# Kernel tuning notes

Hardware: AMD Instinct MI355X
Metric: run time of the kernel (lower is better)

Reference implementation:

```python
import jax, jax.numpy as jnp
import numpy as np


def setup_inputs() -> dict:
    key = jax.random.key(0)
    ks = jax.random.split(key, 8)
    B, L, D = 8, 4096, 1024
    s = 1.0 / np.sqrt(D)  # torch Linear default init scale (approx)
    return {
        "x": jax.random.normal(ks[0], (B, L, D), dtype=jnp.float32),
        "hidden": jax.random.normal(ks[1], (B, D), dtype=jnp.float32),
        "W_f": jax.random.normal(ks[2], (D, D), dtype=jnp.float32) * s,
        "b_f": jnp.zeros((D,), dtype=jnp.float32),
        "W_i": jax.random.normal(ks[3], (D, D), dtype=jnp.float32) * s,
        "b_i": jnp.zeros((D,), dtype=jnp.float32),
        "W_o": jax.random.normal(ks[4], (D, D), dtype=jnp.float32) * s,
        "b_o": jnp.zeros((D,), dtype=jnp.float32),
    }


def reference(x, hidden, W_f, b_f, W_i, b_i, W_o, b_o):
    # x: [B, L, D], hidden: [B, D]
    D = x.shape[-1]
    lin = jnp.linspace(0.0, 1.0, D, dtype=x.dtype)  # per-channel gate scale
    remember = jax.nn.sigmoid(jnp.einsum('bld,ed->ble', x, W_f) + b_f) * lin
    forget = 1.0 - remember
    inp = jnp.tanh(jnp.einsum('bld,ed->ble', x, W_i) + b_i) * remember

    # linear recurrence h_t = forget_t * h_{t-1} + inp_t  via parallel scan
    def combine(c1, c2):
        a1, u1 = c1
        a2, u2 = c2
        return (a1 * a2, a2 * u1 + u2)

    cumprod_forget, h_inner = jax.lax.associative_scan(combine, (forget, inp), axis=1)
    h = h_inner + hidden[:, None, :] * cumprod_forget  # inject initial hidden state
    y = jnp.einsum('bld,ed->ble', h, W_o) + b_o
    return y, h
```

## Files before the change

kernel.cpp:

```cpp
#include <hip/hip_runtime.h>
#include <stdint.h>

#define B_ 8
#define L_ 4096
#define D_ 1024
#define M_ (B_*L_)
#define CHUNKS 128
#define TCH (L_/CHUNKS)

typedef float f32x4 __attribute__((ext_vector_type(4)));
typedef float f32x2 __attribute__((ext_vector_type(2)));
typedef short short8 __attribute__((ext_vector_type(8)));
typedef unsigned short ushort4v __attribute__((ext_vector_type(4)));

static __device__ __forceinline__ unsigned short f2bf(float f) {
  union { float f; unsigned u; } v; v.f = f;
  unsigned r = v.u + 0x7FFFu + ((v.u >> 16) & 1u);
  return (unsigned short)(r >> 16);
}
static __device__ __forceinline__ float bf2f(unsigned short u) {
  union { unsigned u; float f; } v; v.u = ((unsigned)u) << 16; return v.f;
}

#define GLOAD16(g, l) \
  __builtin_amdgcn_global_load_lds((__attribute__((address_space(1))) const void*)(g), \
                                   (__attribute__((address_space(3))) void*)(l), 16, 0, 0)

__global__ __launch_bounds__(256)
void cvt_bf16(const float* __restrict__ src, unsigned short* __restrict__ dst, int n8)
{
  int gid = blockIdx.x * 256 + threadIdx.x;
  if (gid >= n8) return;
  const f32x4* s = (const f32x4*)(src + (size_t)gid * 8);
  f32x4 v0 = s[0], v1 = s[1];
  union { short8 v; unsigned short u[8]; } w;
  w.u[0] = f2bf(v0[0]); w.u[1] = f2bf(v0[1]); w.u[2] = f2bf(v0[2]); w.u[3] = f2bf(v0[3]);
  w.u[4] = f2bf(v1[0]); w.u[5] = f2bf(v1[1]); w.u[6] = f2bf(v1[2]); w.u[7] = f2bf(v1[3]);
  *(short8*)(dst + (size_t)gid * 8) = w.v;
}

__global__ __launch_bounds__(256)
void cvt_w3(const float* __restrict__ w0, const float* __restrict__ w1,
            const float* __restrict__ w2, unsigned short* __restrict__ dst)
{
  const int per = (D_ * D_) / 8 / 256;
  int m = blockIdx.x / per;
  int gid = (blockIdx.x % per) * 256 + threadIdx.x;
  const float* src = (m == 0) ? w0 : (m == 1) ? w1 : w2;
  const f32x4* s = (const f32x4*)(src + (size_t)gid * 8);
  f32x4 v0 = s[0], v1 = s[1];
  union { short8 v; unsigned short u[8]; } w;
  w.u[0] = f2bf(v0[0]); w.u[1] = f2bf(v0[1]); w.u[2] = f2bf(v0[2]); w.u[3] = f2bf(v0[3]);
  w.u[4] = f2bf(v1[0]); w.u[5] = f2bf(v1[1]); w.u[6] = f2bf(v1[2]); w.u[7] = f2bf(v1[3]);
  *(short8*)(dst + (size_t)m * D_ * D_ + (size_t)gid * 8) = w.v;
}

template<int MODE>
__global__ __launch_bounds__(512, 2)
void gemm256(const unsigned short* __restrict__ A,
             const unsigned short* __restrict__ Bw,
             const float* __restrict__ bias0,
             const float* __restrict__ bias1,
             unsigned short* __restrict__ ob0,
             unsigned short* __restrict__ ob1,
             float* __restrict__ of)
{
  __shared__ unsigned short lds[81920];
  char* ldsb = (char*)lds;

  const int tid  = threadIdx.x;
  const int lane = tid & 63;
  const int wid  = tid >> 6;
  const int wm   = wid >> 2;
  const int wn   = wid & 3;
  const int frow = lane & 15, ks = lane >> 4;
  const int xsw  = (ks ^ ((frow >> 1) & 3)) << 4;

  constexpr int NBN = (MODE == 0) ? 8 : 4;
  constexpr int GBM = 32 / NBN;
  const int xcd   = blockIdx.x & 7;
  const int slot  = blockIdx.x >> 3;
  const int local = slot & 31;
  const int wrnd  = slot >> 5;
  const int bm = (xcd * 16 + wrnd * GBM + (local & (GBM - 1))) * 256;
  const int bn = (local / GBM) * 256;

  const int r0  = tid >> 2;
  const int scl = ((tid & 3) ^ ((r0 >> 1) & 3)) << 4;
  const char* pA = (const char*)A  + (size_t)(bm + r0) * 2048 + scl;
  const char* pB = (const char*)Bw + (size_t)(bn + r0) * 2048 + scl;
  const int dst16 = tid * 16;

  f32x4 acc[8][4] = {};
  short8 aq[4], bq[4];

  auto stgA = [&](int c, int sl) {
    const char* s = pA + c * 64;
    char* d = ldsb + sl * 16384 + dst16;
    GLOAD16(s,                      d);
    GLOAD16(s + (size_t)128 * 2048, d + 8192);
  };
  auto stgB = [&](int c, int sl) {
    const char* s = pB + c * 64;
    char* d = ldsb + 81920 + sl * 16384 + dst16;
    GLOAD16(s,                      d);
    GLOAD16(s + (size_t)128 * 2048, d + 8192);
  };
  auto ldAB4 = [&](const char* LA, const char* LB) {
    const char* ab = LA + (wm * 128 + frow) * 64 + xsw;
    const char* bb = LB + (wn * 64 + frow) * 64 + xsw;
    aq[0] = *(const short8*)(ab);
    bq[0] = *(const short8*)(bb);
    bq[1] = *(const short8*)(bb + 1024);
    bq[2] = *(const short8*)(bb + 2048);
    bq[3] = *(const short8*)(bb + 3072);
    aq[1] = *(const short8*)(ab + 1024);
    aq[2] = *(const short8*)(ab + 2048);
    aq[3] = *(const short8*)(ab + 3072);
  };
  auto ldA4 = [&](const char* LA) {
    const char* ab = LA + (wm * 128 + 64 + frow) * 64 + xsw;
    aq[0] = *(const short8*)(ab);
    aq[1] = *(const short8*)(ab + 1024);
    aq[2] = *(const short8*)(ab + 2048);
    aq[3] = *(const short8*)(ab + 3072);
  };
  auto mfma16 = [&](int ih) {
    __builtin_amdgcn_s_setprio(1);
    #pragma unroll
    for (int i2 = 0; i2 < 4; ++i2) {
      #pragma unroll
      for (int j = 0; j < 4; ++j)
        acc[ih * 4 + i2][j] =
          __builtin_amdgcn_mfma_f32_16x16x32_bf16(aq[i2], bq[j], acc[ih * 4 + i2][j], 0, 0, 0);
    }
    __builtin_amdgcn_s_setprio(0);
  };

#define BAR __builtin_amdgcn_s_barrier()
#define WAITV(N) asm volatile("s_waitcnt vmcnt(" #N ")" ::: "memory")
#define DO_CH(c, SL, SG, STG, WN)                                             \
  {                                                                           \
    const char* LA = ldsb + (SL) * 16384;                                     \
    const char* LB = ldsb + 81920 + (SL) * 16384;                             \
    ldAB4(LA, LB);                                                            \
    if (STG) stgA((c) + 4, (SG));                                             \
    mfma16(0);                                                                \
    ldA4(LA);                                                                 \
    if (STG) stgB((c) + 4, (SG));                                             \
    mfma16(1);                                                                \
    WAITV(WN);                                                                \
    BAR;                                                                      \
  }
#define DO_CH_LAST(SL)                                                        \
  {                                                                           \
    const char* LA = ldsb + (SL) * 16384;                                     \
    const char* LB = ldsb + 81920 + (SL) * 16384;                             \
    ldAB4(LA, LB);                                                            \
    mfma16(0);                                                                \
    ldA4(LA);                                                                 \
    mfma16(1);                                                                \
  }

  stgA(0, 0); stgB(0, 0);
  stgA(1, 1); stgB(1, 1);
  stgA(2, 2); stgB(2, 2);
  stgA(3, 3); stgB(3, 3);
  WAITV(12);
  BAR;

  DO_CH( 0, 0, 4, true, 12);
  DO_CH( 1, 1, 0, true, 12);
  DO_CH( 2, 2, 1, true, 12);
  DO_CH( 3, 3, 2, true, 12);
  DO_CH( 4, 4, 3, true, 12);
  DO_CH( 5, 0, 4, true, 12);
  DO_CH( 6, 1, 0, true, 12);
  DO_CH( 7, 2, 1, true, 12);
  DO_CH( 8, 3, 2, true, 12);
  DO_CH( 9, 4, 3, true, 12);
  DO_CH(10, 0, 4, true, 12);
  DO_CH(11, 1, 0, true, 12);
  DO_CH(12, 2, 1, true, 12);
  DO_CH(13, 3, 2, true, 12);
  DO_CH(14, 4, 3, true, 12);
  DO_CH(15, 0, 4, true, 12);
  DO_CH(16, 1, 0, true, 12);
  DO_CH(17, 2, 1, true, 12);
  DO_CH(18, 3, 2, true, 12);
  DO_CH(19, 4, 3, true, 12);
  DO_CH(20, 0, 4, true, 12);
  DO_CH(21, 1, 0, true, 12);
  DO_CH(22, 2, 1, true, 12);
  DO_CH(23, 3, 2, true, 12);
  DO_CH(24, 4, 3, true, 12);
  DO_CH(25, 0, 4, true, 12);
  DO_CH(26, 1, 0, true, 12);
  DO_CH(27, 2, 1, true, 12);
  DO_CH(28, 3, 0, false, 8);
  DO_CH(29, 4, 0, false, 4);
  DO_CH(30, 0, 0, false, 0);
  DO_CH_LAST(1);
#undef DO_CH
#undef DO_CH_LAST
#undef WAITV
#undef BAR

  if constexpr (MODE == 0) {
    const int plane = bn >> 10;
    const int cb    = bn & 1023;
    unsigned short* ob = plane ? ob1 : ob0;
    const float* bs    = plane ? bias1 : bias0;
    float bv[4];
    #pragma unroll
    for (int j = 0; j < 4; ++j) bv[j] = bs[cb + wn * 64 + j * 16 + frow];
    #pragma unroll
    for (int ii = 0; ii < 8; ++ii) {
      int row = bm + wm * 128 + ii * 16 + ks * 4;
      #pragma unroll
      for (int j = 0; j < 4; ++j) {
        int col = cb + wn * 64 + j * 16 + frow;
        float lin = (float)col * (1.0f / 1023.0f);
        #pragma unroll
        for (int r = 0; r < 4; ++r) {
          float z = acc[ii][j][r] + bv[j];
          float v;
          if (plane == 0) {
            v = lin / (1.0f + __expf(-z));
          } else {
            float e2 = __expf(2.0f * z);
            v = 1.0f - 2.0f / (e2 + 1.0f);
          }
          ob[(size_t)(row + r) * D_ + col] = f2bf(v);
        }
      }
    }
  } else {
    float bv[4];
    #pragma unroll
    for (int j = 0; j < 4; ++j) bv[j] = bias0[bn + wn * 64 + j * 16 + frow];
    #pragma unroll
    for (int ii = 0; ii < 8; ++ii) {
      int row = bm + wm * 128 + ii * 16 + ks * 4;
      #pragma unroll
      for (int j = 0; j < 4; ++j) {
        int col = bn + wn * 64 + j * 16 + frow;
        #pragma unroll
        for (int r = 0; r < 4; ++r)
          of[(size_t)(row + r) * D_ + col] = acc[ii][j][r] + bv[j];
      }
    }
  }
}

__global__ __launch_bounds__(256)
void scan_partial_b(const unsigned short* __restrict__ rb,
                    const unsigned short* __restrict__ tb,
                    float* __restrict__ Ag, float* __restrict__ Ug)
{
  int blk = blockIdx.x;
  int b = blk >> 7, c = blk & (CHUNKS - 1);
  int e = threadIdx.x << 2;
  size_t base = ((size_t)b * L_ + (size_t)c * TCH) * D_ + e;
  f32x4 a = {1.f,1.f,1.f,1.f}, u = {0.f,0.f,0.f,0.f};
  for (int t = 0; t < TCH; ++t) {
    ushort4v r4 = *(const ushort4v*)(rb + base + (size_t)t * D_);
    ushort4v t4 = *(const ushort4v*)(tb + base + (size_t)t * D_);
    #pragma unroll
    for (int j = 0; j < 4; ++j) {
      float rem = bf2f(r4[j]);
      float f   = 1.0f - rem;
      float inp = bf2f(t4[j]) * rem;
      u[j] = fmaf(f, u[j], inp);
      a[j] *= f;
    }
  }
  size_t o = (size_t)(b * CHUNKS + c) * D_ + e;
  *(f32x4*)(Ag + o) = a;
  *(f32x4*)(Ug + o) = u;
}

__global__ __launch_bounds__(256)
void scan_carry(const float* __restrict__ Ag, const float* __restrict__ Ug,
                const float* __restrict__ hidden, float* __restrict__ Hin)
{
  int gid = blockIdx.x * 256 + threadIdx.x;
  int b = gid >> 8;
  int e = (gid & 255) << 2;
  f32x4 h = *(const f32x4*)(hidden + (size_t)b * D_ + e);
  for (int c = 0; c < CHUNKS; ++c) {
    size_t o = (size_t)(b * CHUNKS + c) * D_ + e;
    *(f32x4*)(Hin + o) = h;
    f32x4 A = *(const f32x4*)(Ag + o);
    f32x4 U = *(const f32x4*)(Ug + o);
    h = A * h + U;
  }
}

__global__ __launch_bounds__(256)
void scan_apply_b(const unsigned short* __restrict__ rb,
                  const unsigned short* __restrict__ tb,
                  const float* __restrict__ Hin,
                  float* __restrict__ hout, unsigned short* __restrict__ hb)
{
  int blk = blockIdx.x;
  int b = blk >> 7, c = blk & (CHUNKS - 1);
  int e = threadIdx.x << 2;
  size_t base = ((size_t)b * L_ + (size_t)c * TCH) * D_ + e;
  f32x4 h = *(const f32x4*)(Hin + (size_t)(b * CHUNKS + c) * D_ + e);
  for (int t = 0; t < TCH; ++t) {
    size_t o = base + (size_t)t * D_;
    ushort4v r4 = *(const ushort4v*)(rb + o);
    ushort4v t4 = *(const ushort4v*)(tb + o);
    #pragma unroll
    for (int j = 0; j < 4; ++j) {
      float rem = bf2f(r4[j]);
      float f   = 1.0f - rem;
      float inp = bf2f(t4[j]) * rem;
      h[j] = fmaf(f, h[j], inp);
    }
    *(f32x4*)(hout + o) = h;
    ushort4v p;
    p[0] = f2bf(h[0]); p[1] = f2bf(h[1]); p[2] = f2bf(h[2]); p[3] = f2bf(h[3]);
    *(ushort4v*)(hb + o) = p;
  }
}

template<int MODE>
__global__ __launch_bounds__(256, 2)
void gemm_slow(const float* __restrict__ A, const float* __restrict__ B0,
               const float* __restrict__ B1, const float* __restrict__ bias0,
               const float* __restrict__ bias1, float* __restrict__ out0,
               float* __restrict__ out1)
{
  constexpr int BK = 32;
  __shared__ unsigned short As[128 * BK];
  __shared__ unsigned short Bs0[128 * BK];
  __shared__ unsigned short Bs1[(MODE == 0) ? (128 * BK) : 8];

  const int tid = threadIdx.x, lane = tid & 63, wave = tid >> 6;
  const int wr = wave >> 1, wc = wave & 1;
  const int bm = blockIdx.x * 128, bn = blockIdx.y * 128;
  f32x4 acc0[4][4] = {};
  f32x4 acc1[(MODE == 0) ? 4 : 1][(MODE == 0) ? 4 : 1] = {};
  const int frow = lane & 15, kslot = lane >> 4;
  const int xs = kslot ^ (frow & 3);

  auto stage = [&](const float* src, unsigned short* dst) {
    #pragma unroll
    for (int p = 0; p < 4; ++p) {
      int g = p * 256 + tid;
      int row = g >> 3, kq = (g & 7) << 2;
      f32x4 v = *(const f32x4*)(src + (size_t)row * D_ + kq);
      ushort4v w;
      w[0] = f2bf(v[0]); w[1] = f2bf(v[1]); w[2] = f2bf(v[2]); w[3] = f2bf(v[3]);
      int byte = kq << 1, slot = byte >> 4, sub = byte & 15;
      int off = row * 64 + ((slot ^ (row & 3)) << 4) + sub;
      *(ushort4v*)((char*)dst + off) = w;
    }
  };

  for (int k0 = 0; k0 < D_; k0 += BK) {
    stage(A + (size_t)bm * D_ + k0, As);
    stage(B0 + (size_t)bn * D_ + k0, Bs0);
    if constexpr (MODE == 0) stage(B1 + (size_t)bn * D_ + k0, Bs1);
    __syncthreads();
    short8 af[4], bf0[4], bf1[4];
    #pragma unroll
    for (int i = 0; i < 4; ++i) {
      int ar = wr * 64 + i * 16 + frow;
      af[i] = *(const short8*)((const char*)As + ar * 64 + (xs << 4));
      int br = wc * 64 + i * 16 + frow;
      bf0[i] = *(const short8*)((const char*)Bs0 + br * 64 + (xs << 4));
      if constexpr (MODE == 0)
        bf1[i] = *(const short8*)((const char*)Bs1 + br * 64 + (xs << 4));
    }
    #pragma unroll
    for (int i = 0; i < 4; ++i)
      #pragma unroll
      for (int j = 0; j < 4; ++j) {
        acc0[i][j] = __builtin_amdgcn_mfma_f32_16x16x32_bf16(af[i], bf0[j], acc0[i][j], 0, 0, 0);
        if constexpr (MODE == 0)
          acc1[i][j] = __builtin_amdgcn_mfma_f32_16x16x32_bf16(af[i], bf1[j], acc1[i][j], 0, 0, 0);
      }
    __syncthreads();
  }
  #pragma unroll
  for (int i = 0; i < 4; ++i)
    #pragma unroll
    for (int j = 0; j < 4; ++j)
      #pragma unroll
      for (int r = 0; r < 4; ++r) {
        int row = bm + wr * 64 + i * 16 + (lane >> 4) * 4 + r;
        int col = bn + wc * 64 + j * 16 + (lane & 15);
        size_t idx = (size_t)row * D_ + col;
        if constexpr (MODE == 0) {
          float zf = acc0[i][j][r] + bias0[col];
          float linv = (float)col * (1.0f / 1023.0f);
          float rem = linv / (1.0f + __expf(-zf));
          float zi = acc1[i][j][r] + bias1[col];
          float e2 = __expf(2.0f * zi);
          float th = 1.0f - 2.0f / (e2 + 1.0f);
          out0[idx] = 1.0f - rem;
          out1[idx] = th * rem;
        } else {
          out0[idx] = acc0[i][j][r] + bias0[col];
        }
      }
}

__global__ __launch_bounds__(256)
void scan_partial_f(const float* __restrict__ p0, const float* __restrict__ p1,
                    float* __restrict__ Ag, float* __restrict__ Ug)
{
  int blk = blockIdx.x;
  int b = blk / (CHUNKS * 2);
  int c = (blk >> 1) & (CHUNKS - 1);
  int e = ((blk & 1) << 9) + threadIdx.x * 2;
  size_t base = ((size_t)b * L_ + (size_t)c * TCH) * D_ + e;
  f32x2 a = {1.0f, 1.0f}, u = {0.0f, 0.0f};
  for (int t = 0; t < TCH; ++t) {
    f32x2 f = *(const f32x2*)(p0 + base + (size_t)t * D_);
    f32x2 i = *(const f32x2*)(p1 + base + (size_t)t * D_);
    u = f * u + i;
    a = a * f;
  }
  size_t o = (size_t)(b * CHUNKS + c) * D_ + e;
  *(f32x2*)(Ag + o) = a;
  *(f32x2*)(Ug + o) = u;
}

__global__ __launch_bounds__(256)
void scan_apply_f(const float* __restrict__ p0, float* __restrict__ p1_io,
                  const float* __restrict__ Hin)
{
  int blk = blockIdx.x;
  int b = blk / (CHUNKS * 2);
  int c = (blk >> 1) & (CHUNKS - 1);
  int e = ((blk & 1) << 9) + threadIdx.x * 2;
  size_t base = ((size_t)b * L_ + (size_t)c * TCH) * D_ + e;
  f32x2 h = *(const f32x2*)(Hin + (size_t)(b * CHUNKS + c) * D_ + e);
  for (int t = 0; t < TCH; ++t) {
    size_t o = base + (size_t)t * D_;
    f32x2 f = *(const f32x2*)(p0 + o);
    f32x2 i = *(const f32x2*)(p1_io + o);
    h = f * h + i;
    *(f32x2*)(p1_io + o) = h;
  }
}

extern "C" void kernel_launch(void* const* d_in, const int* in_sizes, int n_in,
                              void* d_out, int out_size, void* d_ws, size_t ws_size,
                              hipStream_t stream)
{
  const float* x      = (const float*)d_in[0];
  const float* hidden = (const float*)d_in[1];
  const float* W_f    = (const float*)d_in[2];
  const float* b_f    = (const float*)d_in[3];
  const float* W_i    = (const float*)d_in[4];
  const float* b_i    = (const float*)d_in[5];
  const float* W_o    = (const float*)d_in[6];
  const float* b_o    = (const float*)d_in[7];

  float* y = (float*)d_out;
  float* h = y + (size_t)M_ * D_;

  const size_t xb_elems = (size_t)M_ * D_;
  const size_t w_elems  = (size_t)D_ * D_;
  const size_t agg      = (size_t)B_ * CHUNKS * D_;
  const size_t need = (xb_elems * 3 + 3 * w_elems) * 2 + agg * 3 * 4;

  if (ws_size >= need) {
    unsigned short* xb  = (unsigned short*)d_ws;
    unsigned short* wfb = xb + xb_elems;
    unsigned short* wib = wfb + w_elems;
    unsigned short* wob = wib + w_elems;
    unsigned short* rbv = wob + w_elems;
    unsigned short* tbv = rbv + xb_elems;
    float* Ag  = (float*)(tbv + xb_elems);
    float* Ug  = Ag + agg;
    float* Hin = Ug + agg;

    cvt_bf16<<<(int)(xb_elems / 8 / 256), 256, 0, stream>>>(x, xb, (int)(xb_elems / 8));
    cvt_w3<<<3 * (int)(w_elems / 8 / 256), 256, 0, stream>>>(W_f, W_i, W_o, wfb);

    gemm256<0><<<1024, 512, 0, stream>>>(xb, wfb, b_f, b_i, rbv, tbv, nullptr);

    int pblocks = B_ * CHUNKS;
    scan_partial_b<<<pblocks, 256, 0, stream>>>(rbv, tbv, Ag, Ug);
    scan_carry<<<(B_ * D_ / 4) / 256, 256, 0, stream>>>(Ag, Ug, hidden, Hin);
    scan_apply_b<<<pblocks, 256, 0, stream>>>(rbv, tbv, Hin, h, xb);

    gemm256<1><<<512, 512, 0, stream>>>(xb, wob, b_o, nullptr, nullptr, nullptr, y);
  } else {
    float* Ag  = (float*)d_ws;
    float* Ug  = Ag + agg;
    float* Hin = Ug + agg;
    dim3 gg(M_ / 128, D_ / 128);
    int pblocks = B_ * CHUNKS * 2;

    gemm_slow<0><<<gg, 256, 0, stream>>>(x, W_f, W_i, b_f, b_i, y, h);
    scan_partial_f<<<pblocks, 256, 0, stream>>>(y, h, Ag, Ug);
    scan_carry<<<(B_ * D_ / 4) / 256, 256, 0, stream>>>(Ag, Ug, hidden, Hin);
    scan_apply_f<<<pblocks, 256, 0, stream>>>(y, h, Hin);
    gemm_slow<1><<<gg, 256, 0, stream>>>(h, W_o, nullptr, b_o, nullptr, y, nullptr);
  }
}
```

Baseline: 386.6 us.

## Switch GEMM inner loop from 16x16x32 to 32x32x16 bf16 MFMA

```diff
diff --git a/kernel.cpp b/kernel.cpp
--- a/kernel.cpp
+++ b/kernel.cpp
@@ -10,6 +10,7 @@
 
 typedef float f32x4 __attribute__((ext_vector_type(4)));
 typedef float f32x2 __attribute__((ext_vector_type(2)));
+typedef float f32x16 __attribute__((ext_vector_type(16)));
 typedef short short8 __attribute__((ext_vector_type(8)));
 typedef unsigned short ushort4v __attribute__((ext_vector_type(4)));
 
@@ -73,8 +74,8 @@
   const int wid  = tid >> 6;
   const int wm   = wid >> 2;
   const int wn   = wid & 3;
-  const int frow = lane & 15, ks = lane >> 4;
-  const int xsw  = (ks ^ ((frow >> 1) & 3)) << 4;
+  const int r32  = lane & 31;
+  const int ks2  = lane >> 5;
 
   constexpr int NBN = (MODE == 0) ? 8 : 4;
   constexpr int GBM = 32 / NBN;
@@ -91,8 +92,9 @@
   const char* pB = (const char*)Bw + (size_t)(bn + r0) * 2048 + scl;
   const int dst16 = tid * 16;
 
-  f32x4 acc[8][4] = {};
-  short8 aq[4], bq[4];
+  f32x16 acc[4][2] = {};
+  short8 bq00, bq01, bq10, bq11;
+  short8 aqA0, aqA1, aqB0, aqB1;
 
   auto stgA = [&](int c, int sl) {
     const char* s = pA + c * 64;
@@ -106,36 +108,35 @@
     GLOAD16(s,                      d);
     GLOAD16(s + (size_t)128 * 2048, d + 8192);
   };
-  auto ldAB4 = [&](const char* LA, const char* LB) {
-    const char* ab = LA + (wm * 128 + frow) * 64 + xsw;
-    const char* bb = LB + (wn * 64 + frow) * 64 + xsw;
-    aq[0] = *(const short8*)(ab);
-    bq[0] = *(const short8*)(bb);
-    bq[1] = *(const short8*)(bb + 1024);
-    bq[2] = *(const short8*)(bb + 2048);
-    bq[3] = *(const short8*)(bb + 3072);
-    aq[1] = *(const short8*)(ab + 1024);
-    aq[2] = *(const short8*)(ab + 2048);
-    aq[3] = *(const short8*)(ab + 3072);
+
+  auto ldA = [&](const char* LA, int i, short8& d0, short8& d1) {
+    int row = wm * 128 + i * 32 + r32;
+    const char* rb = LA + row * 64;
+    int x = (row >> 1) & 3;
+    d0 = *(const short8*)(rb + (((ks2)     ^ x) << 4));
+    d1 = *(const short8*)(rb + (((2 + ks2) ^ x) << 4));
   };
-  auto ldA4 = [&](const char* LA) {
-    const char* ab = LA + (wm * 128 + 64 + frow) * 64 + xsw;
-    aq[0] = *(const short8*)(ab);
-    aq[1] = *(const short8*)(ab + 1024);
-    aq[2] = *(const short8*)(ab + 2048);
-    aq[3] = *(const short8*)(ab + 3072);
+  auto ldB = [&](const char* LB) {
+    int rowb = wn * 64 + r32;
+    const char* rb0 = LB + rowb * 64;
+    const char* rb1 = LB + (rowb + 32) * 64;
+    int x0 = (rowb >> 1) & 3;
+    int x1 = ((rowb + 32) >> 1) & 3;
+    bq00 = *(const short8*)(rb0 + (((ks2)     ^ x0) << 4));
+    bq01 = *(const short8*)(rb0 + (((2 + ks2) ^ x0) << 4));
+    bq10 = *(const short8*)(rb1 + (((ks2)     ^ x1) << 4));
+    bq11 = *(const short8*)(rb1 + (((2 + ks2) ^ x1) << 4));
   };
-  auto mfma16 = [&](int ih) {
-    __builtin_amdgcn_s_setprio(1);
-    #pragma unroll
-    for (int i2 = 0; i2 < 4; ++i2) {
-      #pragma unroll
-      for (int j = 0; j < 4; ++j)
-        acc[ih * 4 + i2][j] =
-          __builtin_amdgcn_mfma_f32_16x16x32_bf16(aq[i2], bq[j], acc[ih * 4 + i2][j], 0, 0, 0);
-    }
-    __builtin_amdgcn_s_setprio(0);
-  };
+
+#define MFMA4(i, a0, a1)                                                      \
+  {                                                                           \
+    __builtin_amdgcn_s_setprio(1);                                            \
+    acc[i][0] = __builtin_amdgcn_mfma_f32_32x32x16_bf16(a0, bq00, acc[i][0], 0, 0, 0); \
+    acc[i][1] = __builtin_amdgcn_mfma_f32_32x32x16_bf16(a0, bq10, acc[i][1], 0, 0, 0); \
+    acc[i][0] = __builtin_amdgcn_mfma_f32_32x32x16_bf16(a1, bq01, acc[i][0], 0, 0, 0); \
+    acc[i][1] = __builtin_amdgcn_mfma_f32_32x32x16_bf16(a1, bq11, acc[i][1], 0, 0, 0); \
+    __builtin_amdgcn_s_setprio(0);                                            \
+  }
 
 #define BAR __builtin_amdgcn_s_barrier()
 #define WAITV(N) asm volatile("s_waitcnt vmcnt(" #N ")" ::: "memory")
@@ -143,23 +144,19 @@
   {                                                                           \
     const char* LA = ldsb + (SL) * 16384;                                     \
     const char* LB = ldsb + 81920 + (SL) * 16384;                             \
-    ldAB4(LA, LB);                                                            \
+    ldB(LB);                                                                  \
+    ldA(LA, 0, aqA0, aqA1);                                                   \
     if (STG) stgA((c) + 4, (SG));                                             \
-    mfma16(0);                                                                \
-    ldA4(LA);                                                                 \
+    ldA(LA, 1, aqB0, aqB1);                                                   \
+    MFMA4(0, aqA0, aqA1);                                                     \
+    ldA(LA, 2, aqA0, aqA1);                                                   \
+    MFMA4(1, aqB0, aqB1);                                                     \
     if (STG) stgB((c) + 4, (SG));                                             \
-    mfma16(1);                                                                \
+    ldA(LA, 3, aqB0, aqB1);                                                   \
+    MFMA4(2, aqA0, aqA1);                                                     \
+    MFMA4(3, aqB0, aqB1);                                                     \
     WAITV(WN);                                                                \
     BAR;                                                                      \
-  }
-#define DO_CH_LAST(SL)                                                        \
-  {                                                                           \
-    const char* LA = ldsb + (SL) * 16384;                                     \
-    const char* LB = ldsb + 81920 + (SL) * 16384;                             \
-    ldAB4(LA, LB);                                                            \
-    mfma16(0);                                                                \
-    ldA4(LA);                                                                 \
-    mfma16(1);                                                                \
   }
 
   stgA(0, 0); stgB(0, 0);
@@ -200,9 +197,21 @@
   DO_CH(28, 3, 0, false, 8);
   DO_CH(29, 4, 0, false, 4);
   DO_CH(30, 0, 0, false, 0);
-  DO_CH_LAST(1);
+  {
+    const char* LA = ldsb + 1 * 16384;
+    const char* LB = ldsb + 81920 + 1 * 16384;
+    ldB(LB);
+    ldA(LA, 0, aqA0, aqA1);
+    ldA(LA, 1, aqB0, aqB1);
+    MFMA4(0, aqA0, aqA1);
+    ldA(LA, 2, aqA0, aqA1);
+    MFMA4(1, aqB0, aqB1);
+    ldA(LA, 3, aqB0, aqB1);
+    MFMA4(2, aqA0, aqA1);
+    MFMA4(3, aqB0, aqB1);
+  }
 #undef DO_CH
-#undef DO_CH_LAST
+#undef MFMA4
 #undef WAITV
 #undef BAR
 
@@ -211,19 +220,18 @@
     const int cb    = bn & 1023;
     unsigned short* ob = plane ? ob1 : ob0;
     const float* bs    = plane ? bias1 : bias0;
-    float bv[4];
-    #pragma unroll
-    for (int j = 0; j < 4; ++j) bv[j] = bs[cb + wn * 64 + j * 16 + frow];
-    #pragma unroll
-    for (int ii = 0; ii < 8; ++ii) {
-      int row = bm + wm * 128 + ii * 16 + ks * 4;
+    #pragma unroll
+    for (int i = 0; i < 4; ++i) {
+      int rbase = bm + wm * 128 + i * 32 + 4 * ks2;
       #pragma unroll
-      for (int j = 0; j < 4; ++j) {
-        int col = cb + wn * 64 + j * 16 + frow;
+      for (int j = 0; j < 2; ++j) {
+        int col = cb + wn * 64 + j * 32 + r32;
+        float bj  = bs[col];
         float lin = (float)col * (1.0f / 1023.0f);
         #pragma unroll
-        for (int r = 0; r < 4; ++r) {
-          float z = acc[ii][j][r] + bv[j];
+        for (int reg = 0; reg < 16; ++reg) {
+          int row = rbase + (reg & 3) + 8 * (reg >> 2);
+          float z = acc[i][j][reg] + bj;
           float v;
           if (plane == 0) {
             v = lin / (1.0f + __expf(-z));
@@ -231,23 +239,23 @@
             float e2 = __expf(2.0f * z);
             v = 1.0f - 2.0f / (e2 + 1.0f);
           }
-          ob[(size_t)(row + r) * D_ + col] = f2bf(v);
+          ob[(size_t)row * D_ + col] = f2bf(v);
         }
       }
     }
   } else {
-    float bv[4];
-    #pragma unroll
-    for (int j = 0; j < 4; ++j) bv[j] = bias0[bn + wn * 64 + j * 16 + frow];
-    #pragma unroll
-    for (int ii = 0; ii < 8; ++ii) {
-      int row = bm + wm * 128 + ii * 16 + ks * 4;
+    #pragma unroll
+    for (int i = 0; i < 4; ++i) {
+      int rbase = bm + wm * 128 + i * 32 + 4 * ks2;
       #pragma unroll
-      for (int j = 0; j < 4; ++j) {
-        int col = bn + wn * 64 + j * 16 + frow;
+      for (int j = 0; j < 2; ++j) {
+        int col = bn + wn * 64 + j * 32 + r32;
+        float bj = bias0[col];
         #pragma unroll
-        for (int r = 0; r < 4; ++r)
-          of[(size_t)(row + r) * D_ + col] = acc[ii][j][r] + bv[j];
+        for (int reg = 0; reg < 16; ++reg) {
+          int row = rbase + (reg & 3) + 8 * (reg >> 2);
+          of[(size_t)row * D_ + col] = acc[i][j][reg] + bj;
+        }
       }
     }
   }
```

Result: slower. 399.0 us (+3.2%).

## Double-buffer LDS fragments in registers to overlap next-chunk reads with MFMAs

Applied to the files above, without the earlier changes.

```diff
diff --git a/kernel.cpp b/kernel.cpp
--- a/kernel.cpp
+++ b/kernel.cpp
@@ -92,7 +92,8 @@
   const int dst16 = tid * 16;
 
   f32x4 acc[8][4] = {};
-  short8 aq[4], bq[4];
+  short8 fA[2][8];
+  short8 fB[2][4];
 
   auto stgA = [&](int c, int sl) {
     const char* s = pA + c * 64;
@@ -106,60 +107,52 @@
     GLOAD16(s,                      d);
     GLOAD16(s + (size_t)128 * 2048, d + 8192);
   };
-  auto ldAB4 = [&](const char* LA, const char* LB) {
-    const char* ab = LA + (wm * 128 + frow) * 64 + xsw;
-    const char* bb = LB + (wn * 64 + frow) * 64 + xsw;
-    aq[0] = *(const short8*)(ab);
-    bq[0] = *(const short8*)(bb);
-    bq[1] = *(const short8*)(bb + 1024);
-    bq[2] = *(const short8*)(bb + 2048);
-    bq[3] = *(const short8*)(bb + 3072);
-    aq[1] = *(const short8*)(ab + 1024);
-    aq[2] = *(const short8*)(ab + 2048);
-    aq[3] = *(const short8*)(ab + 3072);
-  };
-  auto ldA4 = [&](const char* LA) {
-    const char* ab = LA + (wm * 128 + 64 + frow) * 64 + xsw;
-    aq[0] = *(const short8*)(ab);
-    aq[1] = *(const short8*)(ab + 1024);
-    aq[2] = *(const short8*)(ab + 2048);
-    aq[3] = *(const short8*)(ab + 3072);
-  };
-  auto mfma16 = [&](int ih) {
-    __builtin_amdgcn_s_setprio(1);
-    #pragma unroll
-    for (int i2 = 0; i2 < 4; ++i2) {
-      #pragma unroll
-      for (int j = 0; j < 4; ++j)
-        acc[ih * 4 + i2][j] =
-          __builtin_amdgcn_mfma_f32_16x16x32_bf16(aq[i2], bq[j], acc[ih * 4 + i2][j], 0, 0, 0);
-    }
-    __builtin_amdgcn_s_setprio(0);
-  };
+
+#define LDFR(P, SL)                                                           \
+  {                                                                           \
+    const char* LA  = ldsb + (SL) * 16384;                                    \
+    const char* LB  = ldsb + 81920 + (SL) * 16384;                            \
+    const char* ab0 = LA + (wm * 128 + frow) * 64 + xsw;                      \
+    const char* bb  = LB + (wn * 64 + frow) * 64 + xsw;                       \
+    const char* ab1 = LA + (wm * 128 + 64 + frow) * 64 + xsw;                 \
+    fA[P][0] = *(const short8*)(ab0);                                         \
+    fB[P][0] = *(const short8*)(bb);                                          \
+    fB[P][1] = *(const short8*)(bb + 1024);                                   \
+    fB[P][2] = *(const short8*)(bb + 2048);                                   \
+    fB[P][3] = *(const short8*)(bb + 3072);                                   \
+    fA[P][1] = *(const short8*)(ab0 + 1024);                                  \
+    fA[P][2] = *(const short8*)(ab0 + 2048);                                  \
+    fA[P][3] = *(const short8*)(ab0 + 3072);                                  \
+    fA[P][4] = *(const short8*)(ab1);                                         \
+    fA[P][5] = *(const short8*)(ab1 + 1024);                                  \
+    fA[P][6] = *(const short8*)(ab1 + 2048);                                  \
+    fA[P][7] = *(const short8*)(ab1 + 3072);                                  \
+  }
+
+#define MFMA32(P)                                                             \
+  {                                                                           \
+    __builtin_amdgcn_s_setprio(1);                                            \
+    _Pragma("unroll")                                                         \
+    for (int i = 0; i < 4; ++i) {                                             \
+      _Pragma("unroll")                                                       \
+      for (int j = 0; j < 4; ++j) {                                           \
+        acc[i][j]     = __builtin_amdgcn_mfma_f32_16x16x32_bf16(fA[P][i],     fB[P][j], acc[i][j],     0, 0, 0); \
+        acc[4 + i][j] = __builtin_amdgcn_mfma_f32_16x16x32_bf16(fA[P][4 + i], fB[P][j], acc[4 + i][j], 0, 0, 0); \
+      }                                                                       \
+    }                                                                         \
+    __builtin_amdgcn_s_setprio(0);                                            \
+  }
 
 #define BAR __builtin_amdgcn_s_barrier()
 #define WAITV(N) asm volatile("s_waitcnt vmcnt(" #N ")" ::: "memory")
-#define DO_CH(c, SL, SG, STG, WN)                                             \
+#define ITER(SLN, PN, SG, STG, WN, PC)                                        \
   {                                                                           \
-    const char* LA = ldsb + (SL) * 16384;                                     \
-    const char* LB = ldsb + 81920 + (SL) * 16384;                             \
-    ldAB4(LA, LB);                                                            \
-    if (STG) stgA((c) + 4, (SG));                                             \
-    mfma16(0);                                                                \
-    ldA4(LA);                                                                 \
-    if (STG) stgB((c) + 4, (SG));                                             \
-    mfma16(1);                                                                \
     WAITV(WN);                                                                \
     BAR;                                                                      \
-  }
-#define DO_CH_LAST(SL)                                                        \
-  {                                                                           \
-    const char* LA = ldsb + (SL) * 16384;                                     \
-    const char* LB = ldsb + 81920 + (SL) * 16384;                             \
-    ldAB4(LA, LB);                                                            \
-    mfma16(0);                                                                \
-    ldA4(LA);                                                                 \
-    mfma16(1);                                                                \
+    LDFR(PN, SLN);                                                            \
+    if (STG) { stgA(_c4, SG); stgB(_c4, SG); }                                \
+    MFMA32(PC);                                                               \
+    ++_c4;                                                                    \
   }
 
   stgA(0, 0); stgB(0, 0);
@@ -168,41 +161,44 @@
   stgA(3, 3); stgB(3, 3);
   WAITV(12);
   BAR;
-
-  DO_CH( 0, 0, 4, true, 12);
-  DO_CH( 1, 1, 0, true, 12);
-  DO_CH( 2, 2, 1, true, 12);
-  DO_CH( 3, 3, 2, true, 12);
-  DO_CH( 4, 4, 3, true, 12);
-  DO_CH( 5, 0, 4, true, 12);
-  DO_CH( 6, 1, 0, true, 12);
-  DO_CH( 7, 2, 1, true, 12);
-  DO_CH( 8, 3, 2, true, 12);
-  DO_CH( 9, 4, 3, true, 12);
-  DO_CH(10, 0, 4, true, 12);
-  DO_CH(11, 1, 0, true, 12);
-  DO_CH(12, 2, 1, true, 12);
-  DO_CH(13, 3, 2, true, 12);
-  DO_CH(14, 4, 3, true, 12);
-  DO_CH(15, 0, 4, true, 12);
-  DO_CH(16, 1, 0, true, 12);
-  DO_CH(17, 2, 1, true, 12);
-  DO_CH(18, 3, 2, true, 12);
-  DO_CH(19, 4, 3, true, 12);
-  DO_CH(20, 0, 4, true, 12);
-  DO_CH(21, 1, 0, true, 12);
-  DO_CH(22, 2, 1, true, 12);
-  DO_CH(23, 3, 2, true, 12);
-  DO_CH(24, 4, 3, true, 12);
-  DO_CH(25, 0, 4, true, 12);
-  DO_CH(26, 1, 0, true, 12);
-  DO_CH(27, 2, 1, true, 12);
-  DO_CH(28, 3, 0, false, 8);
-  DO_CH(29, 4, 0, false, 4);
-  DO_CH(30, 0, 0, false, 0);
-  DO_CH_LAST(1);
-#undef DO_CH
-#undef DO_CH_LAST
+  LDFR(0, 0);
+
+  int _c4 = 4;
+  ITER(1, 1, 4, true, 8, 0);
+  ITER(2, 0, 0, true, 8, 1);
+  ITER(3, 1, 1, true, 8, 0);
+  ITER(4, 0, 2, true, 8, 1);
+  ITER(0, 1, 3, true, 8, 0);
+  ITER(1, 0, 4, true, 8, 1);
+  ITER(2, 1, 0, true, 8, 0);
+  ITER(3, 0, 1, true, 8, 1);
+  ITER(4, 1, 2, true, 8, 0);
+  ITER(0, 0, 3, true, 8, 1);
+  ITER(1, 1, 4, true, 8, 0);
+  ITER(2, 0, 0, true, 8, 1);
+  ITER(3, 1, 1, true, 8, 0);
+  ITER(4, 0, 2, true, 8, 1);
+  ITER(0, 1, 3, true, 8, 0);
+  ITER(1, 0, 4, true, 8, 1);
+  ITER(2, 1, 0, true, 8, 0);
+  ITER(3, 0, 1, true, 8, 1);
+  ITER(4, 1, 2, true, 8, 0);
+  ITER(0, 0, 3, true, 8, 1);
+  ITER(1, 1, 4, true, 8, 0);
+  ITER(2, 0, 0, true, 8, 1);
+  ITER(3, 1, 1, true, 8, 0);
+  ITER(4, 0, 2, true, 8, 1);
+  ITER(0, 1, 3, true, 8, 0);
+  ITER(1, 0, 4, true, 8, 1);
+  ITER(2, 1, 0, true, 8, 0);
+  ITER(3, 0, 1, true, 8, 1);
+  ITER(4, 1, 0, false, 8, 0);
+  ITER(0, 0, 0, false, 4, 1);
+  ITER(1, 1, 0, false, 0, 0);
+  MFMA32(1);
+#undef ITER
+#undef MFMA32
+#undef LDFR
 #undef WAITV
 #undef BAR
 
```

Result: slower. 398.7 us (+3.1%).
